# Kernel optimization log

Measured on AMD Instinct MI355X. Metric: run time of the kernel, lower is better.

## Reference

```python
import jax, jax.numpy as jnp
import numpy as np

B, N, E, H = 4, 2048, 768, 8
D = E // H
SCALING = D ** (-0.5)


def setup_inputs() -> dict:
    key = jax.random.key(0)
    k0, k1, k2, k3, k4 = jax.random.split(key, 5)
    x = jax.random.normal(k0, (B, N, E), dtype=jnp.float32)
    Wqkv = jax.random.normal(k1, (E, 3 * E), dtype=jnp.float32) * 0.02
    bqkv = jax.random.normal(k2, (3 * E,), dtype=jnp.float32) * 0.02
    Wproj = jax.random.normal(k3, (E, E), dtype=jnp.float32) * 0.02
    bproj = jax.random.normal(k4, (E,), dtype=jnp.float32) * 0.02
    return {"x": x, "Wqkv": Wqkv, "bqkv": bqkv, "Wproj": Wproj, "bproj": bproj}


def reference(x, Wqkv, bqkv, Wproj, bproj):
    b, n, e = x.shape
    h, d = H, E // H
    # QKV projection: [b, n, 3e]
    qkv = x @ Wqkv + bqkv
    # rearrange 'b n (h d qkv) -> qkv b h n d': qkv is the INNERMOST axis
    qkv = qkv.reshape(b, n, h, d, 3)
    q = jnp.transpose(qkv[..., 0], (0, 2, 1, 3))  # [b, h, n, d]
    k = jnp.transpose(qkv[..., 1], (0, 2, 1, 3))
    v = jnp.transpose(qkv[..., 2], (0, 2, 1, 3))
    # unscaled attention scores, softmax, then post-softmax scaling (as in source)
    energy = jnp.einsum('bhqd,bhkd->bhqk', q, k)  # [b, h, n, n]
    att = jax.nn.softmax(energy, axis=-1) * SCALING
    out = jnp.einsum('bhqk,bhkd->bhqd', att, v)   # [b, h, n, d]
    out = jnp.transpose(out, (0, 2, 1, 3)).reshape(b, n, e)
    return out @ Wproj + bproj
```

## Files before the change

kernel.cpp:

```cpp
#include <hip/hip_runtime.h>
#include <cstdint>

#define BB 4
#define SEQ 2048
#define EMB 768
#define NH 8
#define HD 96
#define E3 2304
#define MTOK 8192
#define NROWS 65536
#define KSPLIT 4
#define SCALING 0.10206207261596575f
#define LOG2E 1.44269504f

typedef unsigned short u16;
typedef unsigned int u32;
typedef __bf16 bf16x8 __attribute__((ext_vector_type(8)));
typedef float f32x4 __attribute__((ext_vector_type(4)));
typedef float f32x16 __attribute__((ext_vector_type(16)));

__device__ __forceinline__ u16 f2bf(float f) {
    union { float f; uint32_t u; } c; c.f = f;
    uint32_t u = c.u;
    return (u16)((u + 0x7FFFu + ((u >> 16) & 1u)) >> 16);
}
__device__ __forceinline__ uint32_t pk2(float a, float b) {
    return (uint32_t)f2bf(a) | ((uint32_t)f2bf(b) << 16);
}
__device__ __forceinline__ uint32_t cvtpk(float a, float b) {
    uint32_t r;
    asm("v_cvt_pk_bf16_f32 %0, %1, %2" : "=v"(r) : "v"(a), "v"(b));
    return r;
}
__device__ __forceinline__ float bf2f(u16 h) {
    union { uint32_t u; float f; } c; c.u = ((uint32_t)h) << 16; return c.f;
}
__device__ __forceinline__ float fexp2(float x) {
    return __builtin_amdgcn_exp2f(x);
}
__device__ __forceinline__ void async16(const u16* g, u16* l) {
    __builtin_amdgcn_global_load_lds(
        (const __attribute__((address_space(1))) void*)g,
        (__attribute__((address_space(3))) void*)l, 16, 0, 0);
}


__device__ __forceinline__ void transpose_body(const float* __restrict__ src,
                                               u16* __restrict__ dst,
                                               int ncols, int mode, int j0, int k0,
                                               int tid, float (*T)[65]) {
#pragma unroll
    for (int it = 0; it < 16; ++it) {
        int lin = it * 256 + tid;
        int rr2 = lin >> 6, jj = lin & 63;
        int j = j0 + jj;
        int c;
        if (mode == 0) c = j;
        else if (mode == 1) { int s = j / 768, rr = j % 768; c = (rr / 96) * 288 + (rr % 96) * 3 + s; }
        else { c = (j / 96) * 288 + (j % 96) * 3 + 2; }
        T[rr2][jj] = src[(k0 + rr2) * ncols + c];
    }
    __syncthreads();
#pragma unroll
    for (int it = 0; it < 16; ++it) {
        int lin = it * 256 + tid;
        int jr = lin >> 6, kc = lin & 63;
        dst[(size_t)(j0 + jr) * 768 + k0 + kc] = f2bf(T[kc][jr]);
    }
}

__global__ __launch_bounds__(256) void prep_kernel(const float* __restrict__ x,
                                                   const float* __restrict__ Wqkv,
                                                   const float* __restrict__ Wproj,
                                                   u16* __restrict__ xb,
                                                   u16* __restrict__ wqkT,
                                                   u16* __restrict__ wvr,
                                                   u16* __restrict__ wpt) {
    __shared__ float T[64][65];
    int bid = blockIdx.x, tid = threadIdx.x;
    if (bid < 3072) {
        int i = bid * 256 + tid;
        const float4* s4 = (const float4*)x;
        float4 a = s4[2 * i];
        float4 c = s4[2 * i + 1];
        uint4 o;
        o.x = pk2(a.x, a.y); o.y = pk2(a.z, a.w);
        o.z = pk2(c.x, c.y); o.w = pk2(c.z, c.w);
        ((uint4*)xb)[i] = o;
    } else if (bid < 3360) {
        int t = bid - 3072;
        transpose_body(Wqkv, wqkT, E3, 1, (t % 24) * 64, (t / 24) * 64, tid, T);
    } else if (bid < 3504) {
        int t = bid - 3360;
        transpose_body(Wqkv, wvr, E3, 2, (t % 12) * 64, (t / 12) * 64, tid, T);
    } else {
        int t = bid - 3504;
        transpose_body(Wproj, wpt, EMB, 0, (t % 12) * 64, (t / 12) * 64, tid, T);
    }
}


__device__ __forceinline__ void gemm_tiles(const u16* __restrict__ A,
                                           const u16* __restrict__ Bt,
                                           int m0, int n0, int tid,
                                           u16* As, u16* Bs, f32x4 acc[4][4]) {
    const int lane = tid & 63;
    const int w = tid >> 6;
    const int l15 = lane & 15;
    const int quad = lane >> 4;
    const int wr = (w >> 1) * 64;
    const int wc = (w & 1) * 64;
    const int swz = l15 & 7;
    for (int kb = 0; kb < 768; kb += 64) {
#pragma unroll
        for (int it = 0; it < 4; ++it) {
            int base = (w * 4 + it) * 64;
            int lin = base + lane;
            int row = lin >> 3, cl = lin & 7;
            int cg = cl ^ (row & 7);
            async16(&A[(size_t)(m0 + row) * 768 + kb + cg * 8], &As[base * 8]);
            async16(&Bt[(size_t)(n0 + row) * 768 + kb + cg * 8], &Bs[base * 8]);
        }
        __syncthreads();
#pragma unroll
        for (int ks = 0; ks < 2; ++ks) {
            bf16x8 af[4], bfg[4];
#pragma unroll
            for (int fi = 0; fi < 4; ++fi)
                af[fi] = *(const bf16x8*)&As[(wr + fi * 16 + l15) * 64 + (((ks * 4 + quad) ^ swz) * 8)];
#pragma unroll
            for (int fj = 0; fj < 4; ++fj)
                bfg[fj] = *(const bf16x8*)&Bs[(wc + fj * 16 + l15) * 64 + (((ks * 4 + quad) ^ swz) * 8)];
#pragma unroll
            for (int fi = 0; fi < 4; ++fi)
#pragma unroll
                for (int fj = 0; fj < 4; ++fj)
                    acc[fi][fj] = __builtin_amdgcn_mfma_f32_16x16x32_bf16(af[fi], bfg[fj], acc[fi][fj], 0, 0, 0);
        }
        __syncthreads();
    }
}

__device__ __forceinline__ void gemm_tiles64(const u16* __restrict__ A,
                                             const u16* __restrict__ Bt,
                                             int m0, int n0, int tid,
                                             u16* As, u16* Bs, f32x4 acc[4][2]) {
    const int lane = tid & 63;
    const int w = tid >> 6;
    const int l15 = lane & 15;
    const int quad = lane >> 4;
    const int wr = (w >> 1) * 64;
    const int wc = (w & 1) * 32;
    const int swz = l15 & 7;
    for (int kb = 0; kb < 768; kb += 64) {
#pragma unroll
        for (int it = 0; it < 4; ++it) {
            int base = (w * 4 + it) * 64;
            int lin = base + lane;
            int row = lin >> 3, cl = lin & 7;
            int cg = cl ^ (row & 7);
            async16(&A[(size_t)(m0 + row) * 768 + kb + cg * 8], &As[base * 8]);
        }
#pragma unroll
        for (int it = 0; it < 2; ++it) {
            int base = (w * 2 + it) * 64;
            int lin = base + lane;
            int row = lin >> 3, cl = lin & 7;
            int cg = cl ^ (row & 7);
            async16(&Bt[(size_t)(n0 + row) * 768 + kb + cg * 8], &Bs[base * 8]);
        }
        __syncthreads();
#pragma unroll
        for (int ks = 0; ks < 2; ++ks) {
            bf16x8 af[4], bfg[2];
#pragma unroll
            for (int fi = 0; fi < 4; ++fi)
                af[fi] = *(const bf16x8*)&As[(wr + fi * 16 + l15) * 64 + (((ks * 4 + quad) ^ swz) * 8)];
#pragma unroll
            for (int fj = 0; fj < 2; ++fj)
                bfg[fj] = *(const bf16x8*)&Bs[(wc + fj * 16 + l15) * 64 + (((ks * 4 + quad) ^ swz) * 8)];
#pragma unroll
            for (int fi = 0; fi < 4; ++fi)
#pragma unroll
                for (int fj = 0; fj < 2; ++fj)
                    acc[fi][fj] = __builtin_amdgcn_mfma_f32_16x16x32_bf16(af[fi], bfg[fj], acc[fi][fj], 0, 0, 0);
        }
        __syncthreads();
    }
}

__global__ __launch_bounds__(256) void gemm_qkv_kernel(const u16* __restrict__ xb,
                                                       const u16* __restrict__ wqkT,
                                                       const u16* __restrict__ wvr,
                                                       const float* __restrict__ bqkv,
                                                       u16* __restrict__ qb,
                                                       u16* __restrict__ kg,
                                                       u16* __restrict__ vt) {
    __shared__ __align__(16) u16 As[128 * 64];
    __shared__ __align__(16) u16 Bs[128 * 64];
    int bid = blockIdx.x, tid = threadIdx.x;
    int lane = tid & 63, w = tid >> 6, l15 = lane & 15, quad = lane >> 4;
    if (bid < 768) {
        int n0 = (bid % 12) * 128, m0 = (bid / 12) * 128;
        f32x4 acc[4][4] = {};
        gemm_tiles(xb, wqkT, m0, n0, tid, As, Bs, acc);
        int wr = (w >> 1) * 64, wc = (w & 1) * 64;
#pragma unroll
        for (int fj = 0; fj < 4; ++fj) {
            int j = n0 + wc + fj * 16 + l15;
            int s = j / 768, rr = j % 768;
            int hh = rr / 96, dd = rr % 96;
            float bv = bqkv[hh * 288 + dd * 3 + s];
#pragma unroll
            for (int fi = 0; fi < 4; ++fi) {
#pragma unroll
                for (int r = 0; r < 4; ++r) {
                    int m = m0 + wr + fi * 16 + quad * 4 + r;
                    int b = m >> 11, n = m & 2047;
                    int bh = b * NH + hh;
                    float v = acc[fi][fj][r] + bv;
                    if (s == 0) {
                        qb[((size_t)bh * SEQ + n) * HD + dd] = f2bf(v * LOG2E);
                    } else {
                        int cp = (dd >> 3) ^ (n & 7);
                        kg[((size_t)bh * SEQ + n) * 128 + cp * 8 + (dd & 7)] = f2bf(v);
                    }
                }
            }
        }
    } else {
        int t = bid - 768;
        int n0 = (t % 128) * 64, m0 = (t / 128) * 128;
        f32x4 acc[4][2] = {};
        gemm_tiles64(wvr, xb, m0, n0, tid, As, Bs, acc);
        int wr = (w >> 1) * 64, wc = (w & 1) * 32;
        float bvs[4][4]; int hhs[4][4], dds[4][4];
#pragma unroll
        for (int fi = 0; fi < 4; ++fi)
#pragma unroll
            for (int r = 0; r < 4; ++r) {
                int m = m0 + wr + fi * 16 + quad * 4 + r;
                int hh = m / 96, dd = m % 96;
                hhs[fi][r] = hh; dds[fi][r] = dd;
                bvs[fi][r] = bqkv[hh * 288 + dd * 3 + 2];
            }
#pragma unroll
        for (int fj = 0; fj < 2; ++fj) {
            int n = n0 + wc + fj * 16 + l15;
            int b = n >> 11, nn = n & 2047;
#pragma unroll
            for (int fi = 0; fi < 4; ++fi) {
#pragma unroll
                for (int r = 0; r < 4; ++r) {
                    int dd = dds[fi][r];
                    int kk = (nn & ~63) | ((((nn >> 3) ^ dd) & 7) << 3) | (nn & 7);
                    vt[((size_t)(b * NH + hhs[fi][r]) * HD + dd) * SEQ + kk] =
                        f2bf(acc[fi][fj][r] + bvs[fi][r]);
                }
            }
        }
    }
}

__global__ __launch_bounds__(256) void gemm_proj_kernel(const u16* __restrict__ A,
                                                        const u16* __restrict__ Bt,
                                                        const float* __restrict__ bias,
                                                        float* __restrict__ out) {
    __shared__ __align__(16) u16 As[128 * 64];
    __shared__ __align__(16) u16 Bs[64 * 64];
    int tid = threadIdx.x;
    int n0 = blockIdx.x * 64, m0 = blockIdx.y * 128;
    f32x4 acc[4][2] = {};
    gemm_tiles64(A, Bt, m0, n0, tid, As, Bs, acc);
    int lane = tid & 63, w = tid >> 6, l15 = lane & 15, quad = lane >> 4;
    int wr = (w >> 1) * 64, wc = (w & 1) * 32;
#pragma unroll
    for (int fj = 0; fj < 2; ++fj) {
        int j = n0 + wc + fj * 16 + l15;
        float bv = bias[j];
#pragma unroll
        for (int fi = 0; fi < 4; ++fi) {
#pragma unroll
            for (int r = 0; r < 4; ++r) {
                int m = m0 + wr + fi * 16 + quad * 4 + r;
                out[(size_t)m * 768 + j] = acc[fi][fj][r] + bv;
            }
        }
    }
}

__global__ __launch_bounds__(256, 2) void attn_kernel(const u16* __restrict__ Q,
                                                      const u16* __restrict__ Kg,
                                                      const u16* __restrict__ Vt,
                                                      u16* __restrict__ part,
                                                      float* __restrict__ lpart) {
    __shared__ __align__(16) u16 Ks[64 * 128];
    __shared__ __align__(16) u16 Vs[96 * 64];
    int tid = threadIdx.x;
    int lane = tid & 63, w = tid >> 6;
    int l31 = lane & 31, hf = lane >> 5;
    int swz = l31 & 7;
    int bid = blockIdx.x;
    int qt = bid >> 7;
    int g = bid & 127;
    int bh = g >> 2, kh = g & 3;
    const u16* qp = Q + (size_t)bh * SEQ * HD;
    const u16* kgp = Kg + (size_t)bh * SEQ * 128;
    const u16* vtp = Vt + (size_t)bh * HD * SEQ;
    int qbase = qt * 256 + w * 64;
    int kbase = kh * 512;

    bf16x8 aq[2][6];
#pragma unroll
    for (int j = 0; j < 2; ++j)
#pragma unroll
        for (int dc = 0; dc < 6; ++dc)
            aq[j][dc] = *(const bf16x8*)&qp[(size_t)(qbase + j * 32 + l31) * HD + dc * 16 + hf * 8];

    f32x16 Ot[2][3] = {};
    float lp[2] = {0.f, 0.f};

    for (int kt = 0; kt < 8; ++kt) {
        int k0 = kbase + kt * 64;
#pragma unroll
        for (int it = 0; it < 4; ++it) {
            int cw = w * 4 + it;
            async16(kgp + (size_t)(k0 + cw * 4 + (lane >> 4)) * 128 + (lane & 15) * 8,
                    &Ks[cw * 512]);
        }
#pragma unroll
        for (int it = 0; it < 3; ++it) {
            int vw = w * 3 + it;
            async16(vtp + (size_t)(vw * 8 + (lane >> 3)) * SEQ + k0 + (lane & 7) * 8,
                    &Vs[vw * 512]);
        }
        __syncthreads();

#pragma unroll
        for (int tau = 0; tau < 2; ++tau) {
            f32x16 Sv0 = {}, Sv1 = {};
            __builtin_amdgcn_s_setprio(1);
#pragma unroll
            for (int dc = 0; dc < 6; ++dc) {
                bf16x8 ka = *(const bf16x8*)&Ks[(tau * 32 + l31) * 128 + (((2 * dc + hf) ^ swz) * 8)];
                Sv0 = __builtin_amdgcn_mfma_f32_32x32x16_bf16(ka, aq[0][dc], Sv0, 0, 0, 0);
                Sv1 = __builtin_amdgcn_mfma_f32_32x32x16_bf16(ka, aq[1][dc], Sv1, 0, 0, 0);
            }
            __builtin_amdgcn_s_setprio(0);
            u32 pk[2][4][2];
#pragma unroll
            for (int g2 = 0; g2 < 4; ++g2)
#pragma unroll
                for (int u = 0; u < 2; ++u) {
                    float a0 = fexp2(Sv0[g2 * 4 + 2 * u]);
                    float a1 = fexp2(Sv0[g2 * 4 + 2 * u + 1]);
                    lp[0] += a0 + a1;
                    pk[0][g2][u] = cvtpk(a0, a1);
                    float b0 = fexp2(Sv1[g2 * 4 + 2 * u]);
                    float b1 = fexp2(Sv1[g2 * 4 + 2 * u + 1]);
                    lp[1] += b0 + b1;
                    pk[1][g2][u] = cvtpk(b0, b1);
                }
#pragma unroll
            for (int j = 0; j < 2; ++j)
#pragma unroll
                for (int kc = 0; kc < 2; ++kc)
#pragma unroll
                    for (int u = 0; u < 2; ++u)
                        asm("v_permlane32_swap_b32 %0, %1"
                            : "+v"(pk[j][2 * kc][u]), "+v"(pk[j][2 * kc + 1][u]));
#pragma unroll
            for (int kc = 0; kc < 2; ++kc) {
                union { u32 u[4]; bf16x8 v; } pf0, pf1;
                pf0.u[0] = pk[0][2 * kc][0];     pf0.u[1] = pk[0][2 * kc][1];
                pf0.u[2] = pk[0][2 * kc + 1][0]; pf0.u[3] = pk[0][2 * kc + 1][1];
                pf1.u[0] = pk[1][2 * kc][0];     pf1.u[1] = pk[1][2 * kc][1];
                pf1.u[2] = pk[1][2 * kc + 1][0]; pf1.u[3] = pk[1][2 * kc + 1][1];
                __builtin_amdgcn_s_setprio(1);
#pragma unroll
                for (int t = 0; t < 3; ++t) {
                    bf16x8 va = *(const bf16x8*)&Vs[(t * 32 + l31) * 64 + (((4 * tau + 2 * kc + hf) ^ swz) * 8)];
                    Ot[0][t] = __builtin_amdgcn_mfma_f32_32x32x16_bf16(va, pf0.v, Ot[0][t], 0, 0, 0);
                    Ot[1][t] = __builtin_amdgcn_mfma_f32_32x32x16_bf16(va, pf1.v, Ot[1][t], 0, 0, 0);
                }
                __builtin_amdgcn_s_setprio(0);
            }
        }
        __syncthreads();
    }

    size_t pb = (size_t)kh * NROWS + (size_t)bh * SEQ;
#pragma unroll
    for (int j = 0; j < 2; ++j) {
        int q = qbase + j * 32 + l31;
        float lr = lp[j] + __shfl_xor(lp[j], 32);
        if (hf == 0) lpart[pb + q] = lr;
        size_t rowb = (pb + q) * HD;
#pragma unroll
        for (int t = 0; t < 3; ++t) {
#pragma unroll
            for (int g2 = 0; g2 < 4; ++g2) {
                int d0 = t * 32 + 8 * g2 + 4 * hf;
                uint2 val;
                val.x = pk2(Ot[j][t][g2 * 4 + 0], Ot[j][t][g2 * 4 + 1]);
                val.y = pk2(Ot[j][t][g2 * 4 + 2], Ot[j][t][g2 * 4 + 3]);
                *(uint2*)&part[rowb + d0] = val;
            }
        }
    }
}

__global__ __launch_bounds__(256) void combine_kernel(const u16* __restrict__ part,
                                                      const float* __restrict__ lpart,
                                                      u16* __restrict__ ao) {
    int idx = blockIdx.x * 256 + threadIdx.x;
    int row = idx / 12, ch = idx % 12;
    float l = 0.f;
#pragma unroll
    for (int k = 0; k < KSPLIT; ++k) l += lpart[(size_t)k * NROWS + row];
    float sc = SCALING / l;
    float acc[8] = {};
#pragma unroll
    for (int k = 0; k < KSPLIT; ++k) {
        uint4 pv = *(const uint4*)&part[((size_t)k * NROWS + row) * HD + ch * 8];
        const u16* a = (const u16*)&pv;
#pragma unroll
        for (int i = 0; i < 8; ++i) acc[i] += bf2f(a[i]);
    }
    uint4 o;
    u32* ou = (u32*)&o;
#pragma unroll
    for (int i = 0; i < 4; ++i)
        ou[i] = pk2(acc[2 * i] * sc, acc[2 * i + 1] * sc);
    int bh = row >> 11, n = row & 2047;
    int b = bh >> 3, h = bh & 7;
    *(uint4*)&ao[((size_t)(b * SEQ + n)) * EMB + h * HD + ch * 8] = o;
}


extern "C" void kernel_launch(void* const* d_in, const int* in_sizes, int n_in,
                              void* d_out, int out_size, void* d_ws, size_t ws_size,
                              hipStream_t stream) {
    const float* x     = (const float*)d_in[0];
    const float* Wqkv  = (const float*)d_in[1];
    const float* bqkv  = (const float*)d_in[2];
    const float* Wproj = (const float*)d_in[3];
    const float* bproj = (const float*)d_in[4];
    float* out = (float*)d_out;

    char* p = (char*)d_ws;
    u16*   qb    = (u16*)p;  p += (size_t)NROWS * HD * 2;
    u16*   kg    = (u16*)p;  p += (size_t)NROWS * 128 * 2;
    u16*   vt    = (u16*)p;  p += (size_t)NROWS * HD * 2;
    u16*   ao    = (u16*)p;  p += (size_t)MTOK * EMB * 2;
    u16*   wpt   = (u16*)p;  p += (size_t)EMB * EMB * 2;
    float* lpart = (float*)p; p += (size_t)KSPLIT * NROWS * 4;
    char*  U     = p;
    u16*   xb    = (u16*)U;
    u16*   wqkT  = (u16*)(U + (size_t)MTOK * EMB * 2);
    u16*   wvr   = (u16*)(U + (size_t)MTOK * EMB * 2 + (size_t)1536 * EMB * 2);
    u16*   partb = (u16*)U;

    prep_kernel<<<3648, 256, 0, stream>>>(x, Wqkv, Wproj, xb, wqkT, wvr, wpt);
    gemm_qkv_kernel<<<1536, 256, 0, stream>>>(xb, wqkT, wvr, bqkv, qb, kg, vt);
    attn_kernel<<<8 * 32 * KSPLIT, 256, 0, stream>>>(qb, kg, vt, partb, lpart);
    combine_kernel<<<NROWS * 12 / 256, 256, 0, stream>>>(partb, lpart, ao);
    gemm_proj_kernel<<<dim3(EMB / 64, MTOK / 128), 256, 0, stream>>>(ao, wpt, bproj, out);
}
```

Measured before the change: 234.8 us.

## Split attention block into 8 waves of 32 query rows each

Each attention block now runs 512 threads (8 waves), and each wave handles 32 query rows instead of 64. Per-thread Q fragments, score and output accumulators are halved, and the K/V tile loads are spread across the 8 waves. The aim is to cut register pressure and raise occupancy (launch bounds 512,4) so latency is hidden better. The trade-off is that each K/V fragment read from LDS now feeds only one MFMA instead of two, which doubles LDS read traffic per FLOP.

```diff
diff --git a/kernel.cpp b/kernel.cpp
--- a/kernel.cpp
+++ b/kernel.cpp
@@ -289,7 +289,7 @@
     }
 }
 
-__global__ __launch_bounds__(256, 2) void attn_kernel(const u16* __restrict__ Q,
+__global__ __launch_bounds__(512, 4) void attn_kernel(const u16* __restrict__ Q,
                                                       const u16* __restrict__ Kg,
                                                       const u16* __restrict__ Vt,
                                                       u16* __restrict__ part,
@@ -307,81 +307,70 @@
     const u16* qp = Q + (size_t)bh * SEQ * HD;
     const u16* kgp = Kg + (size_t)bh * SEQ * 128;
     const u16* vtp = Vt + (size_t)bh * HD * SEQ;
-    int qbase = qt * 256 + w * 64;
+    int qbase = qt * 256 + w * 32;
     int kbase = kh * 512;
 
-    bf16x8 aq[2][6];
-#pragma unroll
-    for (int j = 0; j < 2; ++j)
-#pragma unroll
-        for (int dc = 0; dc < 6; ++dc)
-            aq[j][dc] = *(const bf16x8*)&qp[(size_t)(qbase + j * 32 + l31) * HD + dc * 16 + hf * 8];
-
-    f32x16 Ot[2][3] = {};
-    float lp[2] = {0.f, 0.f};
+    bf16x8 aq[6];
+#pragma unroll
+    for (int dc = 0; dc < 6; ++dc)
+        aq[dc] = *(const bf16x8*)&qp[(size_t)(qbase + l31) * HD + dc * 16 + hf * 8];
+
+    f32x16 Ot[3] = {};
+    float lp = 0.f;
 
     for (int kt = 0; kt < 8; ++kt) {
         int k0 = kbase + kt * 64;
 #pragma unroll
-        for (int it = 0; it < 4; ++it) {
-            int cw = w * 4 + it;
+        for (int it = 0; it < 2; ++it) {
+            int cw = w * 2 + it;
             async16(kgp + (size_t)(k0 + cw * 4 + (lane >> 4)) * 128 + (lane & 15) * 8,
                     &Ks[cw * 512]);
         }
 #pragma unroll
-        for (int it = 0; it < 3; ++it) {
-            int vw = w * 3 + it;
-            async16(vtp + (size_t)(vw * 8 + (lane >> 3)) * SEQ + k0 + (lane & 7) * 8,
-                    &Vs[vw * 512]);
+        for (int it = 0; it < 2; ++it) {
+            int vw = it * 8 + w;
+            if (vw < 12)
+                async16(vtp + (size_t)(vw * 8 + (lane >> 3)) * SEQ + k0 + (lane & 7) * 8,
+                        &Vs[vw * 512]);
         }
         __syncthreads();
 
 #pragma unroll
         for (int tau = 0; tau < 2; ++tau) {
-            f32x16 Sv0 = {}, Sv1 = {};
+            f32x16 Sv = {};
             __builtin_amdgcn_s_setprio(1);
 #pragma unroll
             for (int dc = 0; dc < 6; ++dc) {
                 bf16x8 ka = *(const bf16x8*)&Ks[(tau * 32 + l31) * 128 + (((2 * dc + hf) ^ swz) * 8)];
-                Sv0 = __builtin_amdgcn_mfma_f32_32x32x16_bf16(ka, aq[0][dc], Sv0, 0, 0, 0);
-                Sv1 = __builtin_amdgcn_mfma_f32_32x32x16_bf16(ka, aq[1][dc], Sv1, 0, 0, 0);
+                Sv = __builtin_amdgcn_mfma_f32_32x32x16_bf16(ka, aq[dc], Sv, 0, 0, 0);
             }
             __builtin_amdgcn_s_setprio(0);
-            u32 pk[2][4][2];
+            u32 pk[4][2];
 #pragma unroll
             for (int g2 = 0; g2 < 4; ++g2)
 #pragma unroll
                 for (int u = 0; u < 2; ++u) {
-                    float a0 = fexp2(Sv0[g2 * 4 + 2 * u]);
-                    float a1 = fexp2(Sv0[g2 * 4 + 2 * u + 1]);
-                    lp[0] += a0 + a1;
-                    pk[0][g2][u] = cvtpk(a0, a1);
-                    float b0 = fexp2(Sv1[g2 * 4 + 2 * u]);
-                    float b1 = fexp2(Sv1[g2 * 4 + 2 * u + 1]);
-                    lp[1] += b0 + b1;
-                    pk[1][g2][u] = cvtpk(b0, b1);
+                    float a0 = fexp2(Sv[g2 * 4 + 2 * u]);
+                    float a1 = fexp2(Sv[g2 * 4 + 2 * u + 1]);
+                    lp += a0 + a1;
+                    pk[g2][u] = cvtpk(a0, a1);
                 }
 #pragma unroll
-            for (int j = 0; j < 2; ++j)
-#pragma unroll
-                for (int kc = 0; kc < 2; ++kc)
-#pragma unroll
-                    for (int u = 0; u < 2; ++u)
-                        asm("v_permlane32_swap_b32 %0, %1"
-                            : "+v"(pk[j][2 * kc][u]), "+v"(pk[j][2 * kc + 1][u]));
+            for (int kc = 0; kc < 2; ++kc)
+#pragma unroll
+                for (int u = 0; u < 2; ++u)
+                    asm("v_permlane32_swap_b32 %0, %1"
+                        : "+v"(pk[2 * kc][u]), "+v"(pk[2 * kc + 1][u]));
 #pragma unroll
             for (int kc = 0; kc < 2; ++kc) {
-                union { u32 u[4]; bf16x8 v; } pf0, pf1;
-                pf0.u[0] = pk[0][2 * kc][0];     pf0.u[1] = pk[0][2 * kc][1];
-                pf0.u[2] = pk[0][2 * kc + 1][0]; pf0.u[3] = pk[0][2 * kc + 1][1];
-                pf1.u[0] = pk[1][2 * kc][0];     pf1.u[1] = pk[1][2 * kc][1];
-                pf1.u[2] = pk[1][2 * kc + 1][0]; pf1.u[3] = pk[1][2 * kc + 1][1];
+                union { u32 u[4]; bf16x8 v; } pf;
+                pf.u[0] = pk[2 * kc][0];     pf.u[1] = pk[2 * kc][1];
+                pf.u[2] = pk[2 * kc + 1][0]; pf.u[3] = pk[2 * kc + 1][1];
                 __builtin_amdgcn_s_setprio(1);
 #pragma unroll
                 for (int t = 0; t < 3; ++t) {
                     bf16x8 va = *(const bf16x8*)&Vs[(t * 32 + l31) * 64 + (((4 * tau + 2 * kc + hf) ^ swz) * 8)];
-                    Ot[0][t] = __builtin_amdgcn_mfma_f32_32x32x16_bf16(va, pf0.v, Ot[0][t], 0, 0, 0);
-                    Ot[1][t] = __builtin_amdgcn_mfma_f32_32x32x16_bf16(va, pf1.v, Ot[1][t], 0, 0, 0);
+                    Ot[t] = __builtin_amdgcn_mfma_f32_32x32x16_bf16(va, pf.v, Ot[t], 0, 0, 0);
                 }
                 __builtin_amdgcn_s_setprio(0);
             }
@@ -390,10 +379,9 @@
     }
 
     size_t pb = (size_t)kh * NROWS + (size_t)bh * SEQ;
-#pragma unroll
-    for (int j = 0; j < 2; ++j) {
-        int q = qbase + j * 32 + l31;
-        float lr = lp[j] + __shfl_xor(lp[j], 32);
+    {
+        int q = qbase + l31;
+        float lr = lp + __shfl_xor(lp, 32);
         if (hf == 0) lpart[pb + q] = lr;
         size_t rowb = (pb + q) * HD;
 #pragma unroll
@@ -402,8 +390,8 @@
             for (int g2 = 0; g2 < 4; ++g2) {
                 int d0 = t * 32 + 8 * g2 + 4 * hf;
                 uint2 val;
-                val.x = pk2(Ot[j][t][g2 * 4 + 0], Ot[j][t][g2 * 4 + 1]);
-                val.y = pk2(Ot[j][t][g2 * 4 + 2], Ot[j][t][g2 * 4 + 3]);
+                val.x = pk2(Ot[t][g2 * 4 + 0], Ot[t][g2 * 4 + 1]);
+                val.y = pk2(Ot[t][g2 * 4 + 2], Ot[t][g2 * 4 + 3]);
                 *(uint2*)&part[rowb + d0] = val;
             }
         }
@@ -463,7 +451,7 @@
 
     prep_kernel<<<3648, 256, 0, stream>>>(x, Wqkv, Wproj, xb, wqkT, wvr, wpt);
     gemm_qkv_kernel<<<1536, 256, 0, stream>>>(xb, wqkT, wvr, bqkv, qb, kg, vt);
-    attn_kernel<<<8 * 32 * KSPLIT, 256, 0, stream>>>(qb, kg, vt, partb, lpart);
+    attn_kernel<<<8 * 32 * KSPLIT, 512, 0, stream>>>(qb, kg, vt, partb, lpart);
     combine_kernel<<<NROWS * 12 / 256, 256, 0, stream>>>(partb, lpart, ao);
     gemm_proj_kernel<<<dim3(EMB / 64, MTOK / 128), 256, 0, stream>>>(ao, wpt, bproj, out);
 }
```

Result: no change. 238.2 us (+1.5%).
